# Performance work log

Hardware: AMD Instinct MI355X
Metric: run time of the kernel (lower is better)

## Reference

```python
import jax, jax.numpy as jnp
import numpy as np

N_E = 1024
E_DIM = 256
BETA = 0.25
PERSISTENCE = 0.1
B, T = 16, 1024


def setup_inputs() -> dict:
    key = jax.random.key(0)
    k1, k2 = jax.random.split(key)
    z = jax.random.normal(k1, (B, T, E_DIM), dtype=jnp.float32)
    # nn.Embedding(1+n_e, e_dim) init uniform(-1/n_e, 1/n_e)
    emb_weight = jax.random.uniform(k2, (N_E + 1, E_DIM), dtype=jnp.float32,
                                    minval=-1.0 / N_E, maxval=1.0 / N_E)
    return {"z": z, "emb_weight": emb_weight}


def _loss_contrast(z, ind, book):
    # z: (B,T,e), ind: (B,T) int, book: (n_e+1, e)
    z_q = book[ind]                                   # (B,T,e)
    loss_indices = jnp.sum((z - z_q) ** 2, axis=-1)   # (B,T)
    # ||z - book||^2 expanded to avoid the (B,T,n_e+1,e) intermediate
    z_sq = jnp.sum(z * z, axis=-1)                    # (B,T)
    b_sq = jnp.sum(book * book, axis=-1)              # (n_e+1,)
    cross = jnp.einsum('bte,ne->btn', z, book)        # (B,T,n_e+1)
    loss_all = z_sq[..., None] + b_sq[None, None, :] - 2.0 * cross
    lc = jnp.maximum(loss_indices[..., None] - loss_all + 1e-6 / N_E, 0.0)
    return jnp.mean(lc)


def _forward(z, emb_weight):
    zf = z.reshape(-1, E_DIM)
    d = (jnp.sum(zf * zf, axis=1, keepdims=True)
         + jnp.sum(emb_weight * emb_weight, axis=1)
         - 2.0 * (zf @ emb_weight.T)).reshape(B, T, N_E + 1)

    ind0 = jnp.clip(jnp.argmin(d[:, 0, :], axis=1), 0, N_E - 1)  # (B,)

    def step(carry, d_t):
        ind, coe = carry                              # (B,) int, (B,) f32
        d_here = jnp.take_along_axis(d_t, ind[:, None], axis=1)[:, 0]
        ind_next = jnp.minimum(ind + 1, N_E - 1)
        d_next = jnp.take_along_axis(d_t, ind_next[:, None], axis=1)[:, 0]
        stay = d_here <= d_next - coe
        ind_new = jnp.where(stay, ind, ind_next)
        coe_new = jnp.where(stay, coe + PERSISTENCE / N_E, 0.0)
        return (ind_new, coe_new), ind_new

    coe0 = jnp.zeros((B,), jnp.float32)
    _, inds = jax.lax.scan(step, (ind0, coe0), jnp.swapaxes(d[:, 1:, :], 0, 1))
    encoding_indices = jnp.concatenate([ind0[None, :], inds], axis=0).T  # (B,T)

    book_sg = jax.lax.stop_gradient(emb_weight)  # torch uses .data/.detach() everywhere
    z_q_raw = book_sg[encoding_indices]
    z_q = z + jax.lax.stop_gradient(z_q_raw - z)  # straight-through

    # non-legacy: beta * L(z, sg(book)) + L(sg(z), sg(book))
    loss = (BETA * _loss_contrast(z, encoding_indices, book_sg)
            + _loss_contrast(jax.lax.stop_gradient(z), encoding_indices, book_sg))

    v = jnp.max(encoding_indices) - jnp.min(encoding_indices)
    return z_q, loss, encoding_indices, v


def reference(z, emb_weight):
    return _forward(z, emb_weight)
```

## Files before the change

### kernel.cpp

```cpp
#include <hip/hip_runtime.h>

#define N_E   1024
#define EDIM  256
#define BB    16
#define TT    1024
#define NROW  (BB*TT)
#define NCOL  1025
#define NPAD  1152
#define PERS  (0.1f/1024.0f)
#define EPSC  (1e-6f/1024.0f)

#define OUT_LOSS 4194304
#define OUT_IDX  4194305
#define OUT_V    4210689

#define WS_ZB   0ull
#define WS_BBF  8388608ull
#define WS_BSQ  8978432ull
#define WS_E    8983552ull
#define WS_IND  84481024ull
#define WS_PART 84546560ull
#define WS_Q    84612096ull

typedef __attribute__((ext_vector_type(8))) short short8;
typedef __attribute__((ext_vector_type(4))) float floatx4;

__device__ __forceinline__ unsigned short f2bf(float f) {
    unsigned int u = __float_as_uint(f);
    u = (u + 0x7fffu + ((u >> 16) & 1u)) >> 16;
    return (unsigned short)u;
}

__global__ __launch_bounds__(256) void k0_prep(const float* __restrict__ z,
                                               const float* __restrict__ book,
                                               unsigned short* __restrict__ zb,
                                               unsigned short* __restrict__ bb,
                                               float* __restrict__ bsq) {
    int bx = blockIdx.x, tid = threadIdx.x;
    if (bx < 4096) {
        float4 v = ((const float4*)z)[bx * 256 + tid];
        size_t o = ((size_t)bx * 256 + tid) * 4;
        zb[o + 0] = f2bf(v.x); zb[o + 1] = f2bf(v.y);
        zb[o + 2] = f2bf(v.z); zb[o + 3] = f2bf(v.w);
    } else {
        int row = bx - 4096;
        float v = (row < NCOL) ? book[(size_t)row * EDIM + tid] : 0.0f;
        bb[(size_t)row * EDIM + tid] = f2bf(v);
        __shared__ float sd[256];
        sd[tid] = v * v;
        __syncthreads();
        for (int s = 128; s > 0; s >>= 1) { if (tid < s) sd[tid] += sd[tid + s]; __syncthreads(); }
        if (tid == 0) bsq[row] = sd[0];
    }
}

__global__ __launch_bounds__(256) void k1_gemm(const unsigned short* __restrict__ zb,
                                               const unsigned short* __restrict__ bb,
                                               const float* __restrict__ bsq,
                                               float* __restrict__ e) {
    int tid = threadIdx.x;
    int lane = tid & 63, w = tid >> 6;
    int mBase = blockIdx.x * 128 + (w >> 1) * 64;
    int nBase = blockIdx.y * 128 + (w & 1) * 64;
    int r = lane & 15, q = lane >> 4;

    floatx4 acc[4][4];
    #pragma unroll
    for (int i = 0; i < 4; i++)
        #pragma unroll
        for (int j = 0; j < 4; j++) acc[i][j] = (floatx4){0.f, 0.f, 0.f, 0.f};

    const short8* A = (const short8*)zb;
    const short8* Bm = (const short8*)bb;

    #pragma unroll
    for (int ks = 0; ks < 8; ks++) {
        int k8 = ks * 4 + q;
        short8 a[4], b[4];
        #pragma unroll
        for (int i = 0; i < 4; i++) a[i] = A[(size_t)(mBase + i * 16 + r) * 32 + k8];
        #pragma unroll
        for (int j = 0; j < 4; j++) b[j] = Bm[(size_t)(nBase + j * 16 + r) * 32 + k8];
        #pragma unroll
        for (int i = 0; i < 4; i++)
            #pragma unroll
            for (int j = 0; j < 4; j++)
                acc[i][j] = __builtin_amdgcn_mfma_f32_16x16x32_bf16(a[i], b[j], acc[i][j], 0, 0, 0);
    }

    float bsql[4];
    #pragma unroll
    for (int j = 0; j < 4; j++) bsql[j] = bsq[nBase + j * 16 + r];

    #pragma unroll
    for (int i = 0; i < 4; i++)
        #pragma unroll
        for (int rr = 0; rr < 4; rr++) {
            int m = mBase + i * 16 + q * 4 + rr;
            float* erow = e + (size_t)m * NPAD;
            #pragma unroll
            for (int j = 0; j < 4; j++)
                erow[nBase + j * 16 + r] = fmaf(-2.0f, acc[i][j][rr], bsql[j]);
        }
}

__global__ __launch_bounds__(256) void k1b_q(const float* __restrict__ e,
                                             short* __restrict__ q16) {
    int row = blockIdx.x, tid = threadIdx.x;
    const float* er = e + (size_t)row * NPAD;
    short* qr = q16 + (size_t)row * 1024;
    const float QS = 1.0f / PERS;
    #pragma unroll
    for (int i = 0; i < 4; i++) {
        int c = tid + i * 256;
        float a = er[c], bv = er[c + 1];
        float x = (bv - a) * QS;
        int qv = (x >= 0.0f) ? min((int)x, 1023) : -1;
        if (c == 1023) qv = 0;
        qr[c] = (short)qv;
    }
}

__global__ __launch_bounds__(256) void k2a_argmin(const float* __restrict__ z,
                                                  const float* __restrict__ book,
                                                  const float* __restrict__ bsq,
                                                  int* __restrict__ wind) {
    int b = blockIdx.x, tid = threadIdx.x;
    int lane = tid & 63, w = tid >> 6;

    const float4* zr = (const float4*)(z + (size_t)b * TT * EDIM);
    float4 zv = zr[lane];
    float s = zv.x * zv.x + zv.y * zv.y + zv.z * zv.z + zv.w * zv.w;
    #pragma unroll
    for (int off = 32; off; off >>= 1) s += __shfl_xor(s, off, 64);
    float zsq = s;

    float best = 3.4e38f; int bidx = 0;
    for (int wi = w; wi < 17; wi += 4) {
        int n = wi * 64 + lane;
        if (n < NCOL) {
            const float4* br = (const float4*)(book + (size_t)n * EDIM);
            float c0 = 0.f, c1 = 0.f, c2 = 0.f, c3 = 0.f;
            #pragma unroll 8
            for (int k = 0; k < 64; k++) {
                float4 bo = br[k]; float4 za = zr[k];
                c0 = fmaf(za.x, bo.x, c0); c1 = fmaf(za.y, bo.y, c1);
                c2 = fmaf(za.z, bo.z, c2); c3 = fmaf(za.w, bo.w, c3);
            }
            float cr = (c0 + c1) + (c2 + c3);
            float d0 = (zsq + bsq[n]) - 2.0f * cr;
            if (d0 < best || (d0 == best && n < bidx)) { best = d0; bidx = n; }
        }
    }
    #pragma unroll
    for (int off = 32; off; off >>= 1) {
        float ob = __shfl_xor(best, off, 64);
        int   oi = __shfl_xor(bidx, off, 64);
        if (ob < best || (ob == best && oi < bidx)) { best = ob; bidx = oi; }
    }
    __shared__ float sb[4]; __shared__ int si[4];
    if (lane == 0) { sb[w] = best; si[w] = bidx; }
    __syncthreads();
    if (tid != 0) return;

    best = sb[0]; bidx = si[0];
    for (int i = 1; i < 4; i++) {
        float vv = sb[i]; int ii = si[i];
        if (vv < best || (vv == best && ii < bidx)) { best = vv; bidx = ii; }
    }
    wind[(size_t)b * TT] = min(bidx, N_E - 1);
}

__global__ __attribute__((amdgpu_waves_per_eu(1, 1)))
__launch_bounds__(64) void k2b_scan(const short* __restrict__ q16,
                                    int* __restrict__ wind) {
    int b = blockIdx.x, lane = threadIdx.x;
    size_t ibase = (size_t)b * TT;
    int ind = wind[ibase];
    int kk = 0;

    const short* qb = q16 + (size_t)b * TT * 1024;
    int cur[31], nxt[31];

    int cb = min(ind, 960);
    #pragma unroll
    for (int j = 0; j < 31; j++)
        cur[j] = qb[(size_t)(1 + j) * 1024 + cb + lane];

    int t = 1;
    for (int c = 0; c < 33; c++) {
        int cbn = min(ind, 960);
        if (c < 32) {
            #pragma unroll
            for (int j = 0; j < 31; j++) {
                int tn = t + 31 + j; tn = tn < 1024 ? tn : 1023;
                nxt[j] = qb[(size_t)tn * 1024 + cbn + lane];
            }
        }
        int packed = 0;
        #pragma unroll
        for (int j = 0; j < 31; j++) {
            int rel = ind - cb;
            int qv = __builtin_amdgcn_readlane(cur[j], rel);
            bool stay = (kk <= qv);
            int ip1 = ind + 1; ip1 = ip1 < 1023 ? ip1 : 1023;
            ind = stay ? ind : ip1;
            kk  = stay ? kk + 1 : 0;
            packed = (lane == j) ? ind : packed;
        }
        if (lane < 31) wind[ibase + t + lane] = packed;
        #pragma unroll
        for (int j = 0; j < 31; j++) cur[j] = nxt[j];
        cb = cbn;
        t += 31;
    }
}

__global__ __launch_bounds__(256) void k3_loss_zq(const float* __restrict__ e,
                                                  const int* __restrict__ wind,
                                                  const float* __restrict__ book,
                                                  float* __restrict__ part,
                                                  float* __restrict__ out) {
    int rIdx = blockIdx.x, tid = threadIdx.x;
    int ind = wind[rIdx];
    const float* er = e + (size_t)rIdx * NPAD;
    float eind = er[ind];
    float p = 0.0f;
    for (int n = tid; n < NCOL; n += 256) {
        float v = eind - er[n] + EPSC;
        p += v > 0.0f ? v : 0.0f;
    }
    __shared__ float sd[256];
    sd[tid] = p; __syncthreads();
    for (int s = 128; s > 0; s >>= 1) { if (tid < s) sd[tid] += sd[tid + s]; __syncthreads(); }
    if (tid == 0) { part[rIdx] = sd[0]; out[OUT_IDX + rIdx] = (float)ind; }
    out[(size_t)rIdx * 256 + tid] = book[(size_t)ind * EDIM + tid];
}

__global__ __launch_bounds__(256) void k4_final(const float* __restrict__ part,
                                                const int* __restrict__ wind,
                                                float* __restrict__ out) {
    int tid = threadIdx.x;
    float s = 0.0f;
    for (int i = tid; i < NROW; i += 256) s += part[i];
    __shared__ float sd[256];
    sd[tid] = s; __syncthreads();
    for (int st = 128; st > 0; st >>= 1) { if (tid < st) sd[tid] += sd[tid + st]; __syncthreads(); }
    if (tid == 0) {
        int mn = wind[0], mx = wind[TT - 1];
        for (int b = 1; b < BB; b++) {
            mn = min(mn, wind[(size_t)b * TT]);
            mx = max(mx, wind[(size_t)b * TT + TT - 1]);
        }
        out[OUT_LOSS] = 1.25f * sd[0] / ((float)NROW * (float)NCOL);
        out[OUT_V] = (float)(mx - mn);
    }
}

extern "C" void kernel_launch(void* const* d_in, const int* in_sizes, int n_in,
                              void* d_out, int out_size, void* d_ws, size_t ws_size,
                              hipStream_t stream) {
    const float* z    = (const float*)d_in[0];
    const float* book = (const float*)d_in[1];
    char* ws = (char*)d_ws;
    unsigned short* zb = (unsigned short*)(ws + WS_ZB);
    unsigned short* bb = (unsigned short*)(ws + WS_BBF);
    float* bsq  = (float*)(ws + WS_BSQ);
    float* e    = (float*)(ws + WS_E);
    int*   wind = (int*)(ws + WS_IND);
    float* part = (float*)(ws + WS_PART);
    short* q16  = (short*)(ws + WS_Q);
    float* out  = (float*)d_out;

    hipLaunchKernelGGL(k0_prep,    dim3(4096 + 1152), dim3(256), 0, stream, z, book, zb, bb, bsq);
    hipLaunchKernelGGL(k1_gemm,    dim3(128, 9),      dim3(256), 0, stream, zb, bb, bsq, e);
    hipLaunchKernelGGL(k1b_q,      dim3(NROW),        dim3(256), 0, stream, e, q16);
    hipLaunchKernelGGL(k2a_argmin, dim3(16),          dim3(256), 0, stream, z, book, bsq, wind);
    hipLaunchKernelGGL(k2b_scan,   dim3(16),          dim3(64),  0, stream, q16, wind);
    hipLaunchKernelGGL(k3_loss_zq, dim3(16384),       dim3(256), 0, stream, e, wind, book, part, out);
    hipLaunchKernelGGL(k4_final,   dim3(1),           dim3(256), 0, stream, part, wind, out);
}
```

Measured before the change: 269.8 us.

## Triple-buffer sequential scan with smaller chunks and relative-index tracking

Restructures the per-batch sequential index scan from double-buffered 31-step chunks into a three-buffer rotation of 21-step chunks, so loads are issued two chunks ahead and have more time to land before they are consumed. The index is tracked relative to the window base, which removes a subtraction from the serial dependency chain inside the readlane loop. The window-base prediction is made from a state two chunks old, which could misalign if the index moves more than about 42 positions, and there is added clamping logic and register pressure from three buffers.

```diff
diff --git a/kernel.cpp b/kernel.cpp
--- a/kernel.cpp
+++ b/kernel.cpp
@@ -171,48 +171,63 @@
     wind[(size_t)b * TT] = min(bidx, N_E - 1);
 }
 
+#define CH 21
+#define SCAN_PHASE(CUR, LD, CBCUR, CBLD, CBNXT, CHUNK)                       \
+  {                                                                          \
+    const int chunk_ = (CHUNK);                                              \
+    const int tbase_ = 1 + chunk_ * CH;                                      \
+    int nb_ = CBCUR + rel; nb_ = nb_ < 960 ? nb_ : 960;                      \
+    if (chunk_ + 2 <= 48) {                                                  \
+      const int tl_ = tbase_ + 2 * CH;                                       \
+      _Pragma("unroll")                                                      \
+      for (int j = 0; j < CH; j++) {                                         \
+        int tn_ = tl_ + j; tn_ = tn_ < 1024 ? tn_ : 1023;                    \
+        LD[j] = qb[(size_t)tn_ * 1024 + nb_ + lane];                         \
+      }                                                                      \
+      CBLD = nb_;                                                            \
+    }                                                                        \
+    int packed_ = 0;                                                         \
+    _Pragma("unroll")                                                        \
+    for (int j = 0; j < CH; j++) {                                           \
+      bool live_ = (tbase_ + j) < 1024;                                      \
+      int qv_ = __builtin_amdgcn_readlane(CUR[j], rel);                      \
+      bool stay_ = (kk <= qv_);                                              \
+      int relp_ = rel + 1; relp_ = relp_ < 63 ? relp_ : 63;                  \
+      int rel_n_ = stay_ ? rel : relp_;                                      \
+      int kk_n_ = stay_ ? kk + 1 : 0;                                        \
+      rel = live_ ? rel_n_ : rel;                                            \
+      kk = live_ ? kk_n_ : kk;                                               \
+      packed_ = (lane == j) ? (CBCUR + rel) : packed_;                       \
+    }                                                                        \
+    if (lane < CH && tbase_ + lane < 1024)                                   \
+      wind[ibase + tbase_ + lane] = packed_;                                 \
+    rel = CBCUR + rel - CBNXT;                                               \
+    rel = rel < 0 ? 0 : (rel > 63 ? 63 : rel);                               \
+  }
+
 __global__ __attribute__((amdgpu_waves_per_eu(1, 1)))
 __launch_bounds__(64) void k2b_scan(const short* __restrict__ q16,
                                     int* __restrict__ wind) {
     int b = blockIdx.x, lane = threadIdx.x;
     size_t ibase = (size_t)b * TT;
-    int ind = wind[ibase];
+    int ind0 = wind[ibase];
+    const short* qb = q16 + (size_t)b * TT * 1024;
+
+    int bA[CH], bB[CH], bC[CH];
+    int cb0 = min(ind0, 960);
+    int cbA = cb0, cbB = cb0, cbC = cb0;
+    int rel = ind0 - cb0;
     int kk = 0;
 
-    const short* qb = q16 + (size_t)b * TT * 1024;
-    int cur[31], nxt[31];
-
-    int cb = min(ind, 960);
-    #pragma unroll
-    for (int j = 0; j < 31; j++)
-        cur[j] = qb[(size_t)(1 + j) * 1024 + cb + lane];
-
-    int t = 1;
-    for (int c = 0; c < 33; c++) {
-        int cbn = min(ind, 960);
-        if (c < 32) {
-            #pragma unroll
-            for (int j = 0; j < 31; j++) {
-                int tn = t + 31 + j; tn = tn < 1024 ? tn : 1023;
-                nxt[j] = qb[(size_t)tn * 1024 + cbn + lane];
-            }
-        }
-        int packed = 0;
-        #pragma unroll
-        for (int j = 0; j < 31; j++) {
-            int rel = ind - cb;
-            int qv = __builtin_amdgcn_readlane(cur[j], rel);
-            bool stay = (kk <= qv);
-            int ip1 = ind + 1; ip1 = ip1 < 1023 ? ip1 : 1023;
-            ind = stay ? ind : ip1;
-            kk  = stay ? kk + 1 : 0;
-            packed = (lane == j) ? ind : packed;
-        }
-        if (lane < 31) wind[ibase + t + lane] = packed;
-        #pragma unroll
-        for (int j = 0; j < 31; j++) cur[j] = nxt[j];
-        cb = cbn;
-        t += 31;
+    #pragma unroll
+    for (int j = 0; j < CH; j++) bA[j] = qb[(size_t)(1 + j) * 1024 + cb0 + lane];
+    #pragma unroll
+    for (int j = 0; j < CH; j++) bB[j] = qb[(size_t)(1 + CH + j) * 1024 + cb0 + lane];
+
+    for (int cc = 0; cc < 51; cc += 3) {
+        SCAN_PHASE(bA, bC, cbA, cbC, cbB, cc);
+        SCAN_PHASE(bB, bA, cbB, cbA, cbC, cc + 1);
+        SCAN_PHASE(bC, bB, cbC, cbB, cbA, cc + 2);
     }
 }
 
```

After: 273.0 us. Within noise of the previous version (+1.2%).
